# Performance work log

Measured on AMD Instinct MI355X. Metric: run time of the kernel, lower is better.

The kernel has to match this reference:

```python
import jax, jax.numpy as jnp
import numpy as np

N = 120_000      # points
D = 64           # voxel grid resolution per axis
HID = 96         # hidden_dim
IN = 96          # input_dim
C = HID + IN     # 192, conv input channels
EPS = 1e-5       # BatchNorm eps


def _build_geometry(rng):
    """Precompute the hash-map lookups torchsparse builds on the fly."""
    pts = rng.uniform(0, D - 1e-3, size=(N, 3)).astype(np.float32)
    vox = np.floor(pts).astype(np.int64)                      # voxel coord per point
    flat = (vox[:, 0] * D + vox[:, 1]) * D + vox[:, 2]
    uniq, seg = np.unique(flat, return_inverse=True)          # occupied voxels
    M = uniq.shape[0]
    lut = -np.ones(D * D * D, dtype=np.int64)
    lut[uniq] = np.arange(M)
    ux, uy, uz = uniq // (D * D), (uniq // D) % D, uniq % D
    # 27 kernel offsets for the 3x3x3 sparse conv
    offs = np.array([(dx, dy, dz) for dx in (-1, 0, 1)
                     for dy in (-1, 0, 1) for dz in (-1, 0, 1)], dtype=np.int64)
    nx = ux[:, None] + offs[None, :, 0]
    ny = uy[:, None] + offs[None, :, 1]
    nz = uz[:, None] + offs[None, :, 2]
    ok = (nx >= 0) & (nx < D) & (ny >= 0) & (ny < D) & (nz >= 0) & (nz < D)
    nflat = (np.clip(nx, 0, D - 1) * D + np.clip(ny, 0, D - 1)) * D + np.clip(nz, 0, D - 1)
    nbr = np.where(ok, lut[nflat], -1)
    nbr = np.where(nbr < 0, M, nbr).astype(np.int32)          # row M = zero pad
    # 8 trilinear corners for devoxelization
    frac = pts - vox
    coffs = np.array([(a, b, c) for a in (0, 1) for b in (0, 1) for c in (0, 1)], dtype=np.int64)
    cx = vox[:, 0:1] + coffs[None, :, 0]
    cy = vox[:, 1:2] + coffs[None, :, 1]
    cz = vox[:, 2:3] + coffs[None, :, 2]
    okc = (cx < D) & (cy < D) & (cz < D)
    cflat = (np.clip(cx, 0, D - 1) * D + np.clip(cy, 0, D - 1)) * D + np.clip(cz, 0, D - 1)
    cidx = np.where(okc, lut[cflat], -1)
    w = np.ones((N, 8), dtype=np.float32)
    for k in range(8):
        for d in range(3):
            w[:, k] *= frac[:, d] if coffs[k, d] == 1 else (1.0 - frac[:, d])
    w = np.where(cidx >= 0, w, 0.0).astype(np.float32)        # missing voxel -> weight 0
    cidx = np.where(cidx < 0, M, cidx).astype(np.int32)
    return seg.astype(np.int32), nbr, cidx, w


def setup_inputs() -> dict:
    rng = np.random.default_rng(0)
    seg, nbr, cidx, cw = _build_geometry(rng)
    key = jax.random.key(0)
    ks = jax.random.split(key, 4)
    return {
        "hidden_F": jax.random.normal(ks[0], (N, HID), jnp.float32),
        "query_F": jax.random.normal(ks[1], (N, IN), jnp.float32),
        "W_conv": jax.random.normal(ks[2], (27, C, HID), jnp.float32) * (1.0 / np.sqrt(27.0 * C)),
        "gamma": jnp.ones((HID,), jnp.float32),
        "beta": jnp.zeros((HID,), jnp.float32),
        "W_lin": jax.random.normal(ks[3], (C, IN), jnp.float32) * (1.0 / np.sqrt(C)),
        "b_lin": jnp.zeros((IN,), jnp.float32),
        "corner_w": jnp.asarray(cw),
        "seg_ids": jnp.asarray(seg),
        "nbr_idx": jnp.asarray(nbr),
        "corner_idx": jnp.asarray(cidx),
    }


def reference(hidden_F, query_F, W_conv, gamma, beta, W_lin, b_lin, corner_w,
              seg_ids, nbr_idx, corner_idx):
    M = nbr_idx.shape[0]
    hx = jnp.concatenate([hidden_F, query_F], axis=1)                  # [N, C]
    # initial_voxelize: scatter-mean point features into occupied voxels
    vsum = jax.ops.segment_sum(hx, seg_ids, num_segments=M)            # [M, C]
    cnt = jax.ops.segment_sum(jnp.ones((hx.shape[0], 1), hx.dtype),
                              seg_ids, num_segments=M)
    vfeat = vsum / jnp.maximum(cnt, 1.0)
    # sparse 3x3x3 conv: gather 27 hashed neighbors (row M is zero pad)
    vpad = jnp.concatenate([vfeat, jnp.zeros((1, C), vfeat.dtype)], axis=0)
    acc = jnp.zeros((M, HID), vfeat.dtype)
    for k in range(27):  # fixed small kernel loop
        acc = acc + vpad[nbr_idx[:, k]] @ W_conv[k]
    # BatchNorm (batch stats over occupied voxels) + ReLU
    mu = jnp.mean(acc, axis=0)
    var = jnp.mean((acc - mu) ** 2, axis=0)
    y = jax.nn.relu(gamma * (acc - mu) * jax.lax.rsqrt(var + EPS) + beta)
    # voxel_to_point(nearest=False): trilinear 8-corner gather
    ypad = jnp.concatenate([y, jnp.zeros((1, HID), y.dtype)], axis=0)
    out = jnp.zeros((hx.shape[0], HID), y.dtype)
    for k in range(8):  # fixed corner loop
        out = out + corner_w[:, k:k + 1] * ypad[corner_idx[:, k]]
    # residual point transform: out.F + Linear(hx.F)
    return out + hx @ W_lin + b_lin
```

## Files before the change

### kernel.cpp

```cpp
#include <hip/hip_runtime.h>
#include <hip/hip_bf16.h>
#include <cstdint>

typedef __bf16 bf16;
typedef __bf16 bf16x8 __attribute__((ext_vector_type(8)));
typedef __bf16 bf16x4 __attribute__((ext_vector_type(4)));
typedef float f32x4 __attribute__((ext_vector_type(4)));
typedef int i32x4 __attribute__((ext_vector_type(4)));

#define HIDC 96
#define CINC 192
#define EPSC 1e-5f

#define STG_B 20480
#define STG_ELEM 10240

__global__ void k_repack(const float* __restrict__ Wc, const float* __restrict__ Wl,
                         bf16* __restrict__ dst, int total) {
  int t = blockIdx.x * 256 + threadIdx.x;
  if (t >= total) return;
  int off = t / 18432;
  int rem = t - off * 18432;
  int cix = rem >> 9;
  int lane = (rem >> 3) & 63;
  int j = rem & 7;
  int k = (cix / 6) * 32 + ((lane >> 4) << 3) + j;
  int col = (cix % 6) * 16 + (lane & 15);
  const float* src = (off < 27) ? (Wc + ((size_t)off * CINC + k) * HIDC + col)
                                : (Wl + (size_t)k * HIDC + col);
  int half = (cix >= 18) ? 1 : 0;
  size_t de = (size_t)(off * 2 + half) * STG_ELEM + (size_t)(rem - half * 9216);
  dst[de] = (bf16)(*src);
}

__global__ void k_count(const int* __restrict__ seg, int* __restrict__ cnt, int Npts) {
  int t = blockIdx.x * 256 + threadIdx.x;
  if (t < Npts) atomicAdd(cnt + seg[t], 1);
}

__global__ void k_bsum(const int* __restrict__ cnt, int* __restrict__ bsum, int M) {
  __shared__ int sm[256];
  int i = blockIdx.x * 256 + threadIdx.x;
  sm[threadIdx.x] = (i < M) ? cnt[i] : 0;
  __syncthreads();
  for (int st = 128; st > 0; st >>= 1) {
    if (threadIdx.x < st) sm[threadIdx.x] += sm[threadIdx.x + st];
    __syncthreads();
  }
  if (threadIdx.x == 0) bsum[blockIdx.x] = sm[0];
}

__global__ void k_bscan(int* __restrict__ bsum, int nb) {
  int i = threadIdx.x;
  int v = (i < nb) ? bsum[i] : 0;
  int x = v;
#pragma unroll
  for (int d = 1; d < 64; d <<= 1) {
    int t = __shfl_up(x, d);
    if ((i & 63) >= d) x += t;
  }
  __shared__ int wsum[16];
  if ((i & 63) == 63) wsum[i >> 6] = x;
  __syncthreads();
  if (i < 16) {
    int w = wsum[i];
    int y = w;
#pragma unroll
    for (int d = 1; d < 16; d <<= 1) {
      int t = __shfl_up(y, d, 16);
      if (i >= d) y += t;
    }
    wsum[i] = y - w;
  }
  __syncthreads();
  if (i < nb) bsum[i] = (x - v) + wsum[i >> 6];
}

__global__ void k_ptr(const int* __restrict__ cnt, const int* __restrict__ bsum,
                      int* __restrict__ ptr, int* __restrict__ cursor, int M) {
  __shared__ int sm[256];
  int i = blockIdx.x * 256 + threadIdx.x;
  int v = (i < M) ? cnt[i] : 0;
  sm[threadIdx.x] = v;
  __syncthreads();
  for (int st = 1; st < 256; st <<= 1) {
    int t = (threadIdx.x >= st) ? sm[threadIdx.x - st] : 0;
    __syncthreads();
    sm[threadIdx.x] += t;
    __syncthreads();
  }
  if (i < M) {
    int e = bsum[blockIdx.x] + sm[threadIdx.x] - v;
    ptr[i] = e;
    cursor[i] = e;
  }
}

__global__ void k_scatter(const int* __restrict__ seg, int* __restrict__ cursor,
                          int* __restrict__ plist, int Npts) {
  int t = blockIdx.x * 256 + threadIdx.x;
  if (t < Npts) {
    int pos = atomicAdd(cursor + seg[t], 1);
    plist[pos] = t;
  }
}

__global__ void k_gmean(const float* __restrict__ hid, const float* __restrict__ qry,
                        const int* __restrict__ ptr, const int* __restrict__ cnt,
                        const int* __restrict__ plist, bf16* __restrict__ vpad, int M) {
  int t = blockIdx.x * 256 + threadIdx.x;
  if (t >= (M + 1) * 48) return;
  int v = t / 48;
  int q = t - v * 48;
  f32x4 a = {0.f, 0.f, 0.f, 0.f};
  if (v < M) {
    int st = ptr[v], n = cnt[v];
    const float* base = (q < 24) ? (hid + q * 4) : (qry + (q - 24) * 4);
    for (int j = 0; j < n; j++) {
      int p = plist[st + j];
      a += *(const f32x4*)(base + (size_t)p * HIDC);
    }
    a *= (1.0f / (float)(n > 0 ? n : 1));
  }
  bf16x4 o;
#pragma unroll
  for (int j = 0; j < 4; j++) o[j] = (bf16)a[j];
  *(bf16x4*)(vpad + (size_t)v * CINC + q * 4) = o;
}

__launch_bounds__(256, 3)
__global__ void k_conv(const bf16* __restrict__ vpad, const int* __restrict__ nbr,
                       const bf16* __restrict__ wpack, float* __restrict__ accbuf,
                       float* __restrict__ bnsum, int M, int nblk, int nper) {
  const int bx = (int)(blockIdx.x & 7) * nper + (int)(blockIdx.x >> 3);
  if (bx >= nblk) return;
  __shared__ __align__(16) char smem[40960];
  const int tid = threadIdx.x;
  const int wave = tid >> 6;
  const int lane = tid & 63;
  const int m = lane & 15;
  const int quad = lane >> 4;
  const int rb = bx * 128 + wave * 32;

  f32x4 acc[2][6];
#pragma unroll
  for (int rt = 0; rt < 2; rt++)
#pragma unroll
    for (int ct = 0; ct < 6; ct++) {
      f32x4 z = {0.f, 0.f, 0.f, 0.f};
      acc[rt][ct] = z;
    }

  const char* wb = (const char*)wpack;
  i32x4 breg[5];
#pragma unroll
  for (int i = 0; i < 5; i++)
    breg[i] = *(const i32x4*)(wb + (size_t)(tid + 256 * i) * 16);

  int gidx[2], gidx2[2];
#pragma unroll
  for (int rt = 0; rt < 2; rt++) {
    int r = rb + rt * 16 + m;
    gidx[rt] = (r < M) ? nbr[(size_t)r * 27] : M;
  }
  bf16x8 afn[2][3];
#pragma unroll
  for (int kc2 = 0; kc2 < 3; kc2++)
#pragma unroll
    for (int rt = 0; rt < 2; rt++)
      afn[rt][kc2] = *(const bf16x8*)(vpad + (size_t)gidx[rt] * CINC + kc2 * 32 + quad * 8);

  for (int s = 0; s < 54; s++) {
    const int buf = s & 1;
    {
      char* bbw = smem + (size_t)buf * STG_B;
#pragma unroll
      for (int i = 0; i < 5; i++)
        *(i32x4*)(bbw + (size_t)(tid + 256 * i) * 16) = breg[i];
    }
    __syncthreads();
    if (s < 53) {
      const char* src = wb + (size_t)(s + 1) * STG_B;
#pragma unroll
      for (int i = 0; i < 5; i++)
        breg[i] = *(const i32x4*)(src + (size_t)(tid + 256 * i) * 16);
    }
    bf16x8 afc[2][3];
#pragma unroll
    for (int kc2 = 0; kc2 < 3; kc2++)
#pragma unroll
      for (int rt = 0; rt < 2; rt++) afc[rt][kc2] = afn[rt][kc2];

    const int half = s & 1;
    const int off = s >> 1;
    if (half == 0) {
      const int offn = off + 1;
#pragma unroll
      for (int rt = 0; rt < 2; rt++) {
        int r = rb + rt * 16 + m;
        gidx2[rt] = (r < M && offn < 27) ? nbr[(size_t)r * 27 + offn] : M;
      }
      if (s < 53) {
#pragma unroll
        for (int kc2 = 0; kc2 < 3; kc2++)
#pragma unroll
          for (int rt = 0; rt < 2; rt++)
            afn[rt][kc2] = *(const bf16x8*)(vpad + (size_t)gidx[rt] * CINC +
                                            (kc2 + 3) * 32 + quad * 8);
      }
    } else {
      if (s < 53) {
#pragma unroll
        for (int kc2 = 0; kc2 < 3; kc2++)
#pragma unroll
          for (int rt = 0; rt < 2; rt++)
            afn[rt][kc2] = *(const bf16x8*)(vpad + (size_t)gidx2[rt] * CINC +
                                            kc2 * 32 + quad * 8);
      }
      gidx[0] = gidx2[0];
      gidx[1] = gidx2[1];
    }

    const char* bbr = smem + (size_t)buf * STG_B;
#pragma unroll
    for (int kc2 = 0; kc2 < 3; kc2++) {
#pragma unroll
      for (int ct = 0; ct < 6; ct++) {
        bf16x8 bfm = *(const bf16x8*)(bbr + (size_t)(kc2 * 6 + ct) * 1024 + (size_t)lane * 16);
#pragma unroll
        for (int rt = 0; rt < 2; rt++)
          acc[rt][ct] = __builtin_amdgcn_mfma_f32_16x16x32_bf16(afc[rt][kc2], bfm, acc[rt][ct], 0, 0, 0);
      }
    }
  }

  __syncthreads();

  float ps[6], pq[6];
#pragma unroll
  for (int ct = 0; ct < 6; ct++) { ps[ct] = 0.f; pq[ct] = 0.f; }
#pragma unroll
  for (int rt = 0; rt < 2; rt++)
#pragma unroll
    for (int rr = 0; rr < 4; rr++) {
      const int r2 = rb + rt * 16 + quad * 4 + rr;
      if (r2 < M) {
#pragma unroll
        for (int ct = 0; ct < 6; ct++) {
          float v = acc[rt][ct][rr];
          ps[ct] += v;
          pq[ct] += v * v;
        }
      }
    }
  float* bnp = (float*)(smem + 32768);
  float* bnq = (float*)(smem + 32768 + 4 * 192 * 4 - 0) + 0;
#pragma unroll
  for (int ct = 0; ct < 6; ct++) {
    float s1 = ps[ct], s2 = pq[ct];
    s1 += __shfl_xor(s1, 16);
    s2 += __shfl_xor(s2, 16);
    s1 += __shfl_xor(s1, 32);
    s2 += __shfl_xor(s2, 32);
    if (quad == 0) {
      bnp[wave * 96 + ct * 16 + m] = s1;
      bnp[384 + wave * 96 + ct * 16 + m] = s2;
    }
  }
  (void)bnq;

  float(*trw)[98] = (float(*)[98])(smem + wave * (16 * 98 * 4));
  const int erow = lane >> 3;
  const int ecb = (lane & 7) * 4;
#pragma unroll
  for (int rt = 0; rt < 2; rt++) {
#pragma unroll
    for (int ct = 0; ct < 6; ct++)
#pragma unroll
      for (int rr = 0; rr < 4; rr++)
        trw[quad * 4 + rr][ct * 16 + m] = acc[rt][ct][rr];
#pragma unroll
    for (int rh = 0; rh < 2; rh++) {
      const int row = rh * 8 + erow;
      const int r2 = rb + rt * 16 + row;
      if (r2 < M) {
#pragma unroll
        for (int it = 0; it < 3; it++) {
          f32x4 v = *(const f32x4*)&trw[row][it * 32 + ecb];
          *(f32x4*)(accbuf + (size_t)r2 * HIDC + it * 32 + ecb) = v;
        }
      }
    }
  }

  __syncthreads();
  if (tid < 192) {
    const int which = tid / 96;
    const int c = tid - which * 96;
    const float* basep = bnp + which * 384;
    float s = basep[c] + basep[96 + c] + basep[192 + c] + basep[288 + c];
    atomicAdd(bnsum + which * 96 + c, s);
  }
}

__global__ void k_bnapply(const float* __restrict__ accbuf, const float* __restrict__ bnsum,
                          const float* __restrict__ gamma, const float* __restrict__ beta,
                          bf16* __restrict__ ypad, int M) {
  __shared__ float ssc[96], ssh[96];
  if (threadIdx.x < 96) {
    int c = threadIdx.x;
    float inv = 1.0f / (float)M;
    float mu = bnsum[c] * inv;
    float var = fmaxf(bnsum[96 + c] * inv - mu * mu, 0.f);
    float sc = gamma[c] * rsqrtf(var + EPSC);
    ssc[c] = sc;
    ssh[c] = beta[c] - mu * sc;
  }
  __syncthreads();
  int t = blockIdx.x * 256 + threadIdx.x;
  if (t >= (M + 1) * 12) return;
  int v = t / 12;
  int g = t - v * 12;
  bf16x8 o;
  if (v < M) {
    f32x4 a = *(const f32x4*)(accbuf + (size_t)v * HIDC + g * 8);
    f32x4 b = *(const f32x4*)(accbuf + (size_t)v * HIDC + g * 8 + 4);
#pragma unroll
    for (int j = 0; j < 4; j++) {
      o[j] = (bf16)fmaxf(a[j] * ssc[g * 8 + j] + ssh[g * 8 + j], 0.f);
      o[4 + j] = (bf16)fmaxf(b[j] * ssc[g * 8 + 4 + j] + ssh[g * 8 + 4 + j], 0.f);
    }
  } else {
#pragma unroll
    for (int j = 0; j < 8; j++) o[j] = (bf16)0.f;
  }
  *(bf16x8*)(ypad + (size_t)v * HIDC + g * 8) = o;
}

__launch_bounds__(256, 4)
__global__ void k_linear(const float* __restrict__ hid, const float* __restrict__ qry,
                         const bf16* __restrict__ wlpack, const float* __restrict__ blin,
                         bf16* __restrict__ lin, int Npts) {
  const int tid = threadIdx.x;
  const int wave = tid >> 6;
  const int lane = tid & 63;
  const int m = lane & 15;
  const int quad = lane >> 4;
  const int rb = blockIdx.x * 128 + wave * 32;

  f32x4 acc[2][6];
#pragma unroll
  for (int rt = 0; rt < 2; rt++)
#pragma unroll
    for (int ct = 0; ct < 6; ct++) {
      f32x4 z = {0.f, 0.f, 0.f, 0.f};
      acc[rt][ct] = z;
    }

  int prow[2];
#pragma unroll
  for (int rt = 0; rt < 2; rt++) {
    int r = rb + rt * 16 + m;
    prow[rt] = (r < Npts) ? r : (Npts - 1);
  }
  const char* wp = (const char*)wlpack;
#pragma unroll
  for (int kc = 0; kc < 6; kc++) {
    const float* srcA = (kc < 3) ? (hid + kc * 32) : (qry + (kc - 3) * 32);
    bf16x8 af[2];
#pragma unroll
    for (int rt = 0; rt < 2; rt++) {
      const float* pA = srcA + (size_t)prow[rt] * HIDC + quad * 8;
      f32x4 lo = *(const f32x4*)pA;
      f32x4 hi = *(const f32x4*)(pA + 4);
#pragma unroll
      for (int j = 0; j < 4; j++) {
        af[rt][j] = (bf16)lo[j];
        af[rt][4 + j] = (bf16)hi[j];
      }
    }
    const int half = (kc >= 3) ? 1 : 0;
    const int kcl = kc - half * 3;
#pragma unroll
    for (int ct = 0; ct < 6; ct++) {
      bf16x8 bfm = *(const bf16x8*)(wp + (size_t)half * STG_B +
                                    (size_t)((kcl * 6 + ct) * 64 + lane) * 16);
#pragma unroll
      for (int rt = 0; rt < 2; rt++)
        acc[rt][ct] = __builtin_amdgcn_mfma_f32_16x16x32_bf16(af[rt], bfm, acc[rt][ct], 0, 0, 0);
    }
  }
  float bl[6];
#pragma unroll
  for (int ct = 0; ct < 6; ct++) bl[ct] = blin[ct * 16 + m];
#pragma unroll
  for (int rt = 0; rt < 2; rt++)
#pragma unroll
    for (int rr = 0; rr < 4; rr++) {
      const int r2 = rb + rt * 16 + quad * 4 + rr;
      if (r2 < Npts) {
        bf16* dst = lin + (size_t)r2 * HIDC + m;
#pragma unroll
        for (int ct = 0; ct < 6; ct++)
          dst[ct * 16] = (bf16)(acc[rt][ct][rr] + bl[ct]);
      }
    }
}

__global__ void k_out(const bf16* __restrict__ lin, const bf16* __restrict__ ypad,
                      const float* __restrict__ cw, const int* __restrict__ cidx,
                      float* __restrict__ out, int Npts) {
  int t = blockIdx.x * 256 + threadIdx.x;
  if (t >= Npts * 12) return;
  int p = t / 12;
  int g = t - p * 12;
  float a[8];
  bf16x8 lv = *(const bf16x8*)(lin + (size_t)p * HIDC + g * 8);
#pragma unroll
  for (int j = 0; j < 8; j++) a[j] = (float)lv[j];
  f32x4 w0 = *(const f32x4*)(cw + (size_t)p * 8);
  f32x4 w1 = *(const f32x4*)(cw + (size_t)p * 8 + 4);
  const i32x4* cp = (const i32x4*)(cidx + (size_t)p * 8);
  i32x4 c0 = cp[0], c1 = cp[1];
#pragma unroll
  for (int k = 0; k < 8; k++) {
    int idx = (k < 4) ? c0[k] : c1[k - 4];
    float wk = (k < 4) ? w0[k] : w1[k - 4];
    bf16x8 yv = *(const bf16x8*)(ypad + (size_t)idx * HIDC + g * 8);
#pragma unroll
    for (int j = 0; j < 8; j++) a[j] += wk * (float)yv[j];
  }
  float* op = out + (size_t)p * HIDC + g * 8;
  f32x4 s0, s1;
#pragma unroll
  for (int j = 0; j < 4; j++) { s0[j] = a[j]; s1[j] = a[4 + j]; }
  *(f32x4*)op = s0;
  *(f32x4*)(op + 4) = s1;
}

extern "C" void kernel_launch(void* const* d_in, const int* in_sizes, int n_in,
                              void* d_out, int out_size, void* d_ws, size_t ws_size,
                              hipStream_t stream) {
  const float* hid = (const float*)d_in[0];
  const float* qry = (const float*)d_in[1];
  const float* Wc = (const float*)d_in[2];
  const float* gamma = (const float*)d_in[3];
  const float* beta = (const float*)d_in[4];
  const float* Wl = (const float*)d_in[5];
  const float* blin = (const float*)d_in[6];
  const float* cw = (const float*)d_in[7];
  const int* seg = (const int*)d_in[8];
  const int* nbr = (const int*)d_in[9];
  const int* cidx = (const int*)d_in[10];
  float* out = (float*)d_out;
  const int Npts = in_sizes[0] / HIDC;
  const int M = in_sizes[9] / 27;

  char* ws = (char*)d_ws;
  size_t cur = 0;
  auto alloc = [&](size_t b) { size_t o = cur; cur = (cur + b + 255) & ~(size_t)255; return o; };
  size_t o_cnt = alloc((size_t)M * 4);
  size_t o_bn = alloc(192 * 4);
  size_t zend = cur;
  size_t o_ptr = alloc((size_t)M * 4);
  size_t o_cur = alloc((size_t)M * 4);
  size_t o_pl = alloc((size_t)Npts * 4);
  size_t o_bs = alloc(1024 * 4);
  size_t RA = (size_t)M * HIDC * 4;
  size_t needA = (size_t)Npts * HIDC * 2;
  if (needA > RA) RA = needA;
  size_t o_A = alloc(RA);
  size_t o_B = alloc((size_t)(M + 1) * CINC * 2);
  size_t o_wpack = alloc((size_t)56 * STG_B);
  (void)ws_size; (void)n_in; (void)out_size;

  int* cnt = (int*)(ws + o_cnt);
  float* bnsum = (float*)(ws + o_bn);
  int* ptr = (int*)(ws + o_ptr);
  int* cursor = (int*)(ws + o_cur);
  int* plist = (int*)(ws + o_pl);
  int* bsum = (int*)(ws + o_bs);
  float* accbuf = (float*)(ws + o_A);
  bf16* lin = (bf16*)(ws + o_A);
  bf16* vpad = (bf16*)(ws + o_B);
  bf16* ypad = (bf16*)(ws + o_B);
  bf16* wpack = (bf16*)(ws + o_wpack);
  bf16* wlpack = (bf16*)(ws + o_wpack + (size_t)54 * STG_B);

  hipMemsetAsync(ws, 0, zend, stream);

  int totalRepack = 28 * 18432;
  k_repack<<<(totalRepack + 255) / 256, 256, 0, stream>>>(Wc, Wl, wpack, totalRepack);

  int nb = (M + 255) / 256;
  k_count<<<(Npts + 255) / 256, 256, 0, stream>>>(seg, cnt, Npts);
  k_bsum<<<nb, 256, 0, stream>>>(cnt, bsum, M);
  k_bscan<<<1, 1024, 0, stream>>>(bsum, nb);
  k_ptr<<<nb, 256, 0, stream>>>(cnt, bsum, ptr, cursor, M);
  k_scatter<<<(Npts + 255) / 256, 256, 0, stream>>>(seg, cursor, plist, Npts);
  k_gmean<<<(((M + 1) * 48) + 255) / 256, 256, 0, stream>>>(hid, qry, ptr, cnt, plist, vpad, M);

  int nblk = (M + 127) / 128;
  int nper = (nblk + 7) / 8;
  k_conv<<<nper * 8, 256, 0, stream>>>(vpad, nbr, wpack, accbuf, bnsum, M, nblk, nper);
  k_bnapply<<<((M + 1) * 12 + 255) / 256, 256, 0, stream>>>(accbuf, bnsum, gamma, beta, ypad, M);
  k_linear<<<(Npts + 127) / 128, 256, 0, stream>>>(hid, qry, wlpack, blin, lin, Npts);
  k_out<<<(Npts * 12 + 255) / 256, 256, 0, stream>>>(lin, ypad, cw, cidx, out, Npts);
}
```

Before: 382.2 us.

## Fuse BN-apply, linear and trilinear devoxelize into one kernel

Merges the BatchNorm-apply, residual linear and trilinear-gather kernels into a single kernel. The linear result stays in shared memory instead of making a bf16 round trip through global memory. BN scale/shift and ReLU are now applied on the fly to each gathered fp32 conv output, so the separate ypad tensor is no longer built. The trade-off is that each of the 8 corner gathers now reads fp32 rows, twice the bytes of bf16, and repeats the BN arithmetic per corner. It also relies on the unwritten pad row of accbuf having weight zero, and that row is never zeroed.

```diff
diff --git a/kernel.cpp b/kernel.cpp
--- a/kernel.cpp
+++ b/kernel.cpp
@@ -254,7 +254,6 @@
       }
     }
   float* bnp = (float*)(smem + 32768);
-  float* bnq = (float*)(smem + 32768 + 4 * 192 * 4 - 0) + 0;
 #pragma unroll
   for (int ct = 0; ct < 6; ct++) {
     float s1 = ps[ct], s2 = pq[ct];
@@ -267,7 +266,6 @@
       bnp[384 + wave * 96 + ct * 16 + m] = s2;
     }
   }
-  (void)bnq;
 
   float(*trw)[98] = (float(*)[98])(smem + wave * (16 * 98 * 4));
   const int erow = lane >> 3;
@@ -303,12 +301,18 @@
   }
 }
 
-__global__ void k_bnapply(const float* __restrict__ accbuf, const float* __restrict__ bnsum,
-                          const float* __restrict__ gamma, const float* __restrict__ beta,
-                          bf16* __restrict__ ypad, int M) {
+__launch_bounds__(256, 4)
+__global__ void k_linout(const float* __restrict__ hid, const float* __restrict__ qry,
+                         const bf16* __restrict__ wlpack, const float* __restrict__ blin,
+                         const float* __restrict__ accbuf, const float* __restrict__ bnsum,
+                         const float* __restrict__ gamma, const float* __restrict__ beta,
+                         const float* __restrict__ cw, const int* __restrict__ cidx,
+                         float* __restrict__ out, int Npts, int M) {
+  __shared__ __align__(16) bf16 linT[128][HIDC];
   __shared__ float ssc[96], ssh[96];
-  if (threadIdx.x < 96) {
-    int c = threadIdx.x;
+  const int tid = threadIdx.x;
+  if (tid < 96) {
+    int c = tid;
     float inv = 1.0f / (float)M;
     float mu = bnsum[c] * inv;
     float var = fmaxf(bnsum[96 + c] * inv - mu * mu, 0.f);
@@ -316,32 +320,7 @@
     ssc[c] = sc;
     ssh[c] = beta[c] - mu * sc;
   }
-  __syncthreads();
-  int t = blockIdx.x * 256 + threadIdx.x;
-  if (t >= (M + 1) * 12) return;
-  int v = t / 12;
-  int g = t - v * 12;
-  bf16x8 o;
-  if (v < M) {
-    f32x4 a = *(const f32x4*)(accbuf + (size_t)v * HIDC + g * 8);
-    f32x4 b = *(const f32x4*)(accbuf + (size_t)v * HIDC + g * 8 + 4);
-#pragma unroll
-    for (int j = 0; j < 4; j++) {
-      o[j] = (bf16)fmaxf(a[j] * ssc[g * 8 + j] + ssh[g * 8 + j], 0.f);
-      o[4 + j] = (bf16)fmaxf(b[j] * ssc[g * 8 + 4 + j] + ssh[g * 8 + 4 + j], 0.f);
-    }
-  } else {
-#pragma unroll
-    for (int j = 0; j < 8; j++) o[j] = (bf16)0.f;
-  }
-  *(bf16x8*)(ypad + (size_t)v * HIDC + g * 8) = o;
-}
-
-__launch_bounds__(256, 4)
-__global__ void k_linear(const float* __restrict__ hid, const float* __restrict__ qry,
-                         const bf16* __restrict__ wlpack, const float* __restrict__ blin,
-                         bf16* __restrict__ lin, int Npts) {
-  const int tid = threadIdx.x;
+
   const int wave = tid >> 6;
   const int lane = tid & 63;
   const int m = lane & 15;
@@ -397,45 +376,50 @@
   for (int rt = 0; rt < 2; rt++)
 #pragma unroll
     for (int rr = 0; rr < 4; rr++) {
-      const int r2 = rb + rt * 16 + quad * 4 + rr;
-      if (r2 < Npts) {
-        bf16* dst = lin + (size_t)r2 * HIDC + m;
-#pragma unroll
-        for (int ct = 0; ct < 6; ct++)
-          dst[ct * 16] = (bf16)(acc[rt][ct][rr] + bl[ct]);
-      }
-    }
-}
-
-__global__ void k_out(const bf16* __restrict__ lin, const bf16* __restrict__ ypad,
-                      const float* __restrict__ cw, const int* __restrict__ cidx,
-                      float* __restrict__ out, int Npts) {
-  int t = blockIdx.x * 256 + threadIdx.x;
-  if (t >= Npts * 12) return;
-  int p = t / 12;
-  int g = t - p * 12;
-  float a[8];
-  bf16x8 lv = *(const bf16x8*)(lin + (size_t)p * HIDC + g * 8);
-#pragma unroll
-  for (int j = 0; j < 8; j++) a[j] = (float)lv[j];
-  f32x4 w0 = *(const f32x4*)(cw + (size_t)p * 8);
-  f32x4 w1 = *(const f32x4*)(cw + (size_t)p * 8 + 4);
-  const i32x4* cp = (const i32x4*)(cidx + (size_t)p * 8);
-  i32x4 c0 = cp[0], c1 = cp[1];
-#pragma unroll
-  for (int k = 0; k < 8; k++) {
-    int idx = (k < 4) ? c0[k] : c1[k - 4];
-    float wk = (k < 4) ? w0[k] : w1[k - 4];
-    bf16x8 yv = *(const bf16x8*)(ypad + (size_t)idx * HIDC + g * 8);
-#pragma unroll
-    for (int j = 0; j < 8; j++) a[j] += wk * (float)yv[j];
-  }
-  float* op = out + (size_t)p * HIDC + g * 8;
-  f32x4 s0, s1;
-#pragma unroll
-  for (int j = 0; j < 4; j++) { s0[j] = a[j]; s1[j] = a[4 + j]; }
-  *(f32x4*)op = s0;
-  *(f32x4*)(op + 4) = s1;
+      const int lr = wave * 32 + rt * 16 + quad * 4 + rr;
+#pragma unroll
+      for (int ct = 0; ct < 6; ct++)
+        linT[lr][ct * 16 + m] = (bf16)(acc[rt][ct][rr] + bl[ct]);
+    }
+  __syncthreads();
+
+  const int pbase = blockIdx.x * 128;
+#pragma unroll
+  for (int it = 0; it < 6; it++) {
+    int task = it * 256 + tid;
+    int lp = task / 12;
+    int g = task - lp * 12;
+    int p = pbase + lp;
+    if (p < Npts) {
+      float a[8];
+      bf16x8 lv = *(const bf16x8*)&linT[lp][g * 8];
+#pragma unroll
+      for (int j = 0; j < 8; j++) a[j] = (float)lv[j];
+      f32x4 w0 = *(const f32x4*)(cw + (size_t)p * 8);
+      f32x4 w1 = *(const f32x4*)(cw + (size_t)p * 8 + 4);
+      const i32x4* cp = (const i32x4*)(cidx + (size_t)p * 8);
+      i32x4 c0 = cp[0], c1 = cp[1];
+#pragma unroll
+      for (int k = 0; k < 8; k++) {
+        int idx = (k < 4) ? c0[k] : c1[k - 4];
+        float wk = (k < 4) ? w0[k] : w1[k - 4];
+        const float* base = accbuf + (size_t)idx * HIDC + g * 8;
+        f32x4 v0 = *(const f32x4*)base;
+        f32x4 v1 = *(const f32x4*)(base + 4);
+#pragma unroll
+        for (int j = 0; j < 4; j++) {
+          a[j] += wk * fmaxf(v0[j] * ssc[g * 8 + j] + ssh[g * 8 + j], 0.f);
+          a[4 + j] += wk * fmaxf(v1[j] * ssc[g * 8 + 4 + j] + ssh[g * 8 + 4 + j], 0.f);
+        }
+      }
+      float* op = out + (size_t)p * HIDC + g * 8;
+      f32x4 s0, s1;
+#pragma unroll
+      for (int j = 0; j < 4; j++) { s0[j] = a[j]; s1[j] = a[4 + j]; }
+      *(f32x4*)op = s0;
+      *(f32x4*)(op + 4) = s1;
+    }
+  }
 }
 
 extern "C" void kernel_launch(void* const* d_in, const int* in_sizes, int n_in,
@@ -466,10 +450,7 @@
   size_t o_cur = alloc((size_t)M * 4);
   size_t o_pl = alloc((size_t)Npts * 4);
   size_t o_bs = alloc(1024 * 4);
-  size_t RA = (size_t)M * HIDC * 4;
-  size_t needA = (size_t)Npts * HIDC * 2;
-  if (needA > RA) RA = needA;
-  size_t o_A = alloc(RA);
+  size_t o_A = alloc((size_t)(M + 1) * HIDC * 4);
   size_t o_B = alloc((size_t)(M + 1) * CINC * 2);
   size_t o_wpack = alloc((size_t)56 * STG_B);
   (void)ws_size; (void)n_in; (void)out_size;
@@ -481,9 +462,7 @@
   int* plist = (int*)(ws + o_pl);
   int* bsum = (int*)(ws + o_bs);
   float* accbuf = (float*)(ws + o_A);
-  bf16* lin = (bf16*)(ws + o_A);
   bf16* vpad = (bf16*)(ws + o_B);
-  bf16* ypad = (bf16*)(ws + o_B);
   bf16* wpack = (bf16*)(ws + o_wpack);
   bf16* wlpack = (bf16*)(ws + o_wpack + (size_t)54 * STG_B);
 
@@ -503,7 +482,6 @@
   int nblk = (M + 127) / 128;
   int nper = (nblk + 7) / 8;
   k_conv<<<nper * 8, 256, 0, stream>>>(vpad, nbr, wpack, accbuf, bnsum, M, nblk, nper);
-  k_bnapply<<<((M + 1) * 12 + 255) / 256, 256, 0, stream>>>(accbuf, bnsum, gamma, beta, ypad, M);
-  k_linear<<<(Npts + 127) / 128, 256, 0, stream>>>(hid, qry, wlpack, blin, lin, Npts);
-  k_out<<<(Npts * 12 + 255) / 256, 256, 0, stream>>>(lin, ypad, cw, cidx, out, Npts);
-}
+  k_linout<<<(Npts + 127) / 128, 256, 0, stream>>>(hid, qry, wlpack, blin, accbuf, bnsum,
+                                                   gamma, beta, cw, cidx, out, Npts, M);
+}
```

Result: no change. 377.3 us (-1.3%).
